# Kernel tuning notes

Hardware: AMD Instinct MI355X
Metric: run time of the kernel (lower is better)

Reference implementation:

```python
import jax, jax.numpy as jnp
import numpy as np

B, S, H, NH = 2, 2048, 1024, 16
HD = H // NH  # 64
EPS = 1e-5


def setup_inputs() -> dict:
    key = jax.random.key(0)
    ks = jax.random.split(key, 4)
    return {
        "hidden_states": jax.random.normal(ks[0], (B, S, H), dtype=jnp.float32),
        "W_attn": jax.random.normal(ks[1], (H, 3 * H), dtype=jnp.float32) * (1.0 / np.sqrt(H)),
        "b_attn": jnp.zeros((3 * H,), dtype=jnp.float32),
        "W_proj": jax.random.normal(ks[2], (H, H), dtype=jnp.float32) * (1.0 / np.sqrt(H)),
        "b_proj": jnp.zeros((H,), dtype=jnp.float32),
        "q_gamma": jnp.ones((HD,), dtype=jnp.float32),
        "q_beta": jnp.zeros((HD,), dtype=jnp.float32),
        "k_gamma": jnp.ones((HD,), dtype=jnp.float32),
        "k_beta": jnp.zeros((HD,), dtype=jnp.float32),
    }


def _layernorm(x, gamma, beta):
    mu = jnp.mean(x, axis=-1, keepdims=True)
    var = jnp.mean(jnp.square(x - mu), axis=-1, keepdims=True)
    return (x - mu) * jax.lax.rsqrt(var + EPS) * gamma + beta


def reference(hidden_states, W_attn, b_attn, W_proj, b_proj, q_gamma, q_beta, k_gamma, k_beta):
    b, s, h = hidden_states.shape
    qkv = hidden_states @ W_attn + b_attn  # [B,S,3H]
    q, k, v = jnp.split(qkv, 3, axis=-1)
    # [B,S,H] -> [B,NH,S,HD]
    def to_heads(t):
        return t.reshape(b, s, NH, HD).transpose(0, 2, 1, 3)
    q, k, v = to_heads(q), to_heads(k), to_heads(v)
    # QK LayerNorm over head_dim
    q = _layernorm(q, q_gamma, q_beta)
    k = _layernorm(k, k_gamma, k_beta)
    scale = HD ** (-0.5)
    scores = jnp.einsum("bhqd,bhkd->bhqk", q, k) * scale
    causal = jnp.tril(jnp.ones((s, s), dtype=bool))
    mask_value = jnp.finfo(scores.dtype).min
    scores = jnp.where(causal, scores, mask_value)
    attn = jax.nn.softmax(scores.astype(jnp.float32), axis=-1).astype(q.dtype)
    out = jnp.einsum("bhqk,bhkd->bhqd", attn, v)
    out = out.transpose(0, 2, 1, 3).reshape(b, s, h)
    out = out @ W_proj + b_proj
    return out
```

## Files before the change

### kernel.cpp

```cpp
#include <hip/hip_runtime.h>
#include <hip/hip_bf16.h>

typedef __bf16 bf16x8 __attribute__((ext_vector_type(8)));
typedef float f32x4 __attribute__((ext_vector_type(4)));

#define EPS 1e-5f
#define QSCALE 0.18033688011112042f

__device__ __forceinline__ unsigned short f2bf(float f) {
  union { float f; unsigned int i; } c; c.f = f;
  unsigned int r = c.i + 0x7FFFu + ((c.i >> 16) & 1u);
  return (unsigned short)(r >> 16);
}

__global__ __launch_bounds__(256) void transpose_f32_bf16(
    const float* __restrict__ in, unsigned short* __restrict__ out,
    int R, int C)
{
  __shared__ __align__(16) unsigned short S[64 * 72];
  const int t = threadIdx.x;
  const int r = t >> 2, c4 = (t & 3) * 16;
  const int rt0 = blockIdx.y * 64, ct0 = blockIdx.x * 64;

  {
    long base = (long)(rt0 + r) * C + ct0 + c4;
    float4 a = *(const float4*)&in[base];
    float4 b = *(const float4*)&in[base + 4];
    float4 c = *(const float4*)&in[base + 8];
    float4 d = *(const float4*)&in[base + 12];
    unsigned short v[16] = {f2bf(a.x), f2bf(a.y), f2bf(a.z), f2bf(a.w),
                            f2bf(b.x), f2bf(b.y), f2bf(b.z), f2bf(b.w),
                            f2bf(c.x), f2bf(c.y), f2bf(c.z), f2bf(c.w),
                            f2bf(d.x), f2bf(d.y), f2bf(d.z), f2bf(d.w)};
    *(uint4*)&S[r * 72 + c4]     = *(uint4*)&v[0];
    *(uint4*)&S[r * 72 + c4 + 8] = *(uint4*)&v[8];
  }
  __syncthreads();

  unsigned short tmp[16];
#pragma unroll
  for (int j = 0; j < 16; j++) tmp[j] = S[(c4 + j) * 72 + r];
  *(uint4*)&out[(long)(ct0 + r) * R + rt0 + c4]     = *(uint4*)&tmp[0];
  *(uint4*)&out[(long)(ct0 + r) * R + rt0 + c4 + 8] = *(uint4*)&tmp[8];
}

__global__ __launch_bounds__(256) void convert_f32_bf16(
    const float* __restrict__ in, unsigned short* __restrict__ out)
{
  long i = ((long)blockIdx.x * 256 + threadIdx.x) * 16;
  float4 a = *(const float4*)&in[i];
  float4 b = *(const float4*)&in[i + 4];
  float4 c = *(const float4*)&in[i + 8];
  float4 d = *(const float4*)&in[i + 12];
  unsigned short v[16] = {f2bf(a.x), f2bf(a.y), f2bf(a.z), f2bf(a.w),
                          f2bf(b.x), f2bf(b.y), f2bf(b.z), f2bf(b.w),
                          f2bf(c.x), f2bf(c.y), f2bf(c.z), f2bf(c.w),
                          f2bf(d.x), f2bf(d.y), f2bf(d.z), f2bf(d.w)};
  *(uint4*)&out[i]     = *(uint4*)&v[0];
  *(uint4*)&out[i + 8] = *(uint4*)&v[8];
}

__global__ __launch_bounds__(256) void qkv_ln_kernel(
    const float* __restrict__ Xf,
    const unsigned short* __restrict__ Xbf, int use_xbf,
    const unsigned short* __restrict__ WT,
    const float* __restrict__ bias,
    const float* __restrict__ qg, const float* __restrict__ qb,
    const float* __restrict__ kg, const float* __restrict__ kb,
    unsigned short* __restrict__ Qws, unsigned short* __restrict__ Kws)
{
  __shared__ __align__(16) unsigned short As[2][128 * 32];
  __shared__ __align__(16) unsigned short Bs[2][128 * 32];

  const int tid = threadIdx.x;
  const int w = tid >> 6, lane = tid & 63, quad = lane >> 4, l15 = lane & 15;
  const int mh = w & 1, nh = w >> 1;
  const int n0 = blockIdx.x * 128, m0 = blockIdx.y * 128;

  f32x4 acc[4][4];
#pragma unroll
  for (int i = 0; i < 4; i++)
#pragma unroll
    for (int j = 0; j < 4; j++) acc[i][j] = (f32x4){0.f, 0.f, 0.f, 0.f};

  const int sr2 = tid >> 1, sh2 = (tid & 1) * 16;

  if (use_xbf) {
    long xo = (long)(m0 + sr2) * 1024 + sh2;
    *(uint4*)&As[0][sr2 * 32 + sh2]     = *(const uint4*)&Xbf[xo];
    *(uint4*)&As[0][sr2 * 32 + sh2 + 8] = *(const uint4*)&Xbf[xo + 8];
  } else {
    long xo = (long)(m0 + sr2) * 1024 + sh2;
    float4 a0 = *(const float4*)&Xf[xo];
    float4 a1 = *(const float4*)&Xf[xo + 4];
    float4 a2 = *(const float4*)&Xf[xo + 8];
    float4 a3 = *(const float4*)&Xf[xo + 12];
    unsigned short v[16] = {f2bf(a0.x), f2bf(a0.y), f2bf(a0.z), f2bf(a0.w),
                            f2bf(a1.x), f2bf(a1.y), f2bf(a1.z), f2bf(a1.w),
                            f2bf(a2.x), f2bf(a2.y), f2bf(a2.z), f2bf(a2.w),
                            f2bf(a3.x), f2bf(a3.y), f2bf(a3.z), f2bf(a3.w)};
    *(uint4*)&As[0][sr2 * 32 + sh2]     = *(uint4*)&v[0];
    *(uint4*)&As[0][sr2 * 32 + sh2 + 8] = *(uint4*)&v[8];
  }
  {
    long wo = (long)(n0 + sr2) * 1024 + sh2;
    *(uint4*)&Bs[0][sr2 * 32 + sh2]     = *(const uint4*)&WT[wo];
    *(uint4*)&Bs[0][sr2 * 32 + sh2 + 8] = *(const uint4*)&WT[wo + 8];
  }
  __syncthreads();

  int buf = 0;
  for (int kt = 0; kt < 1024; kt += 32) {
    const int nbuf = buf ^ 1;
    const bool pf = (kt + 32) < 1024;
    uint4 xv0, xv1, wv0, wv1;
    float4 a0, a1, a2, a3;
    if (pf) {
      if (use_xbf) {
        long xo = (long)(m0 + sr2) * 1024 + kt + 32 + sh2;
        xv0 = *(const uint4*)&Xbf[xo];
        xv1 = *(const uint4*)&Xbf[xo + 8];
      } else {
        long xo = (long)(m0 + sr2) * 1024 + kt + 32 + sh2;
        a0 = *(const float4*)&Xf[xo];
        a1 = *(const float4*)&Xf[xo + 4];
        a2 = *(const float4*)&Xf[xo + 8];
        a3 = *(const float4*)&Xf[xo + 12];
      }
      long wo = (long)(n0 + sr2) * 1024 + kt + 32 + sh2;
      wv0 = *(const uint4*)&WT[wo];
      wv1 = *(const uint4*)&WT[wo + 8];
    }

    bf16x8 af[4], bfr[4];
#pragma unroll
    for (int mq = 0; mq < 4; mq++)
      af[mq] = *(const bf16x8*)&As[buf][(mh * 64 + mq * 16 + l15) * 32 + quad * 8];
#pragma unroll
    for (int nq = 0; nq < 4; nq++)
      bfr[nq] = *(const bf16x8*)&Bs[buf][(nh * 64 + nq * 16 + l15) * 32 + quad * 8];
#pragma unroll
    for (int mq = 0; mq < 4; mq++)
#pragma unroll
      for (int nq = 0; nq < 4; nq++)
        acc[mq][nq] = __builtin_amdgcn_mfma_f32_16x16x32_bf16(af[mq], bfr[nq], acc[mq][nq], 0, 0, 0);

    if (pf) {
      if (use_xbf) {
        *(uint4*)&As[nbuf][sr2 * 32 + sh2]     = xv0;
        *(uint4*)&As[nbuf][sr2 * 32 + sh2 + 8] = xv1;
      } else {
        unsigned short v[16] = {f2bf(a0.x), f2bf(a0.y), f2bf(a0.z), f2bf(a0.w),
                                f2bf(a1.x), f2bf(a1.y), f2bf(a1.z), f2bf(a1.w),
                                f2bf(a2.x), f2bf(a2.y), f2bf(a2.z), f2bf(a2.w),
                                f2bf(a3.x), f2bf(a3.y), f2bf(a3.z), f2bf(a3.w)};
        *(uint4*)&As[nbuf][sr2 * 32 + sh2]     = *(uint4*)&v[0];
        *(uint4*)&As[nbuf][sr2 * 32 + sh2 + 8] = *(uint4*)&v[8];
      }
      *(uint4*)&Bs[nbuf][sr2 * 32 + sh2]     = wv0;
      *(uint4*)&Bs[nbuf][sr2 * 32 + sh2 + 8] = wv1;
    }
    __syncthreads();
    buf = nbuf;
  }

#pragma unroll
  for (int nq = 0; nq < 4; nq++) {
    float bv = bias[n0 + nh * 64 + nq * 16 + l15];
#pragma unroll
    for (int mq = 0; mq < 4; mq++)
#pragma unroll
      for (int rr = 0; rr < 4; rr++) acc[mq][nq][rr] += bv;
  }

  const int g = (n0 >> 6) + nh;
  const bool isQ = g < 16;

  {
    float gv[4], bev[4];
#pragma unroll
    for (int nq = 0; nq < 4; nq++) {
      int d = nq * 16 + l15;
      gv[nq]  = isQ ? qg[d] : kg[d];
      bev[nq] = isQ ? qb[d] : kb[d];
      if (isQ) { gv[nq] *= QSCALE; bev[nq] *= QSCALE; }
    }
#pragma unroll
    for (int mq = 0; mq < 4; mq++)
#pragma unroll
      for (int rr = 0; rr < 4; rr++) {
        float s  = acc[mq][0][rr] + acc[mq][1][rr] + acc[mq][2][rr] + acc[mq][3][rr];
        float s2 = acc[mq][0][rr]*acc[mq][0][rr] + acc[mq][1][rr]*acc[mq][1][rr]
                 + acc[mq][2][rr]*acc[mq][2][rr] + acc[mq][3][rr]*acc[mq][3][rr];
#pragma unroll
        for (int off = 1; off < 16; off <<= 1) {
          s  += __shfl_xor(s,  off, 64);
          s2 += __shfl_xor(s2, off, 64);
        }
        float mu   = s * (1.0f / 64.0f);
        float var  = fmaxf(s2 * (1.0f / 64.0f) - mu * mu, 0.f);
        float rstd = rsqrtf(var + EPS);
#pragma unroll
        for (int nq = 0; nq < 4; nq++)
          acc[mq][nq][rr] = (acc[mq][nq][rr] - mu) * rstd * gv[nq] + bev[nq];
      }
  }

  unsigned short* dst = isQ ? Qws : Kws;
  const int head = isQ ? g : g - 16;

#pragma unroll
  for (int mq = 0; mq < 4; mq++)
#pragma unroll
    for (int rr = 0; rr < 4; rr++) {
      int m = m0 + mh * 64 + mq * 16 + quad * 4 + rr;
      int b = m >> 11, s = m & 2047;
      long base = ((long)((b * 16 + head) * 2048 + s)) * 64;
#pragma unroll
      for (int nq = 0; nq < 4; nq++)
        dst[base + nq * 16 + l15] = f2bf(acc[mq][nq][rr]);
    }
}

__global__ __launch_bounds__(256) void vt_kernel(
    const float* __restrict__ Xf,
    const unsigned short* __restrict__ Xbf, int use_xbf,
    const unsigned short* __restrict__ WvT,
    const float* __restrict__ bias,
    unsigned short* __restrict__ Vt)
{
  __shared__ __align__(16) unsigned short As[2][128 * 32];
  __shared__ __align__(16) unsigned short Bs[2][128 * 32];

  const int tid = threadIdx.x;
  const int w = tid >> 6, lane = tid & 63, quad = lane >> 4, l15 = lane & 15;
  const int mh = w & 1, nh = w >> 1;
  const int n0 = blockIdx.x * 128, m0 = blockIdx.y * 128, bz = blockIdx.z;
  const long xrow0 = (long)bz * 2048;

  f32x4 acc[4][4];
#pragma unroll
  for (int i = 0; i < 4; i++)
#pragma unroll
    for (int j = 0; j < 4; j++) acc[i][j] = (f32x4){0.f, 0.f, 0.f, 0.f};

  const int sr2 = tid >> 1, sh2 = (tid & 1) * 16;

  {
    long wo = (long)(m0 + sr2) * 1024 + sh2;
    *(uint4*)&As[0][sr2 * 32 + sh2]     = *(const uint4*)&WvT[wo];
    *(uint4*)&As[0][sr2 * 32 + sh2 + 8] = *(const uint4*)&WvT[wo + 8];
  }
  if (use_xbf) {
    long xo = (xrow0 + n0 + sr2) * 1024 + sh2;
    *(uint4*)&Bs[0][sr2 * 32 + sh2]     = *(const uint4*)&Xbf[xo];
    *(uint4*)&Bs[0][sr2 * 32 + sh2 + 8] = *(const uint4*)&Xbf[xo + 8];
  } else {
    long xo = (xrow0 + n0 + sr2) * 1024 + sh2;
    float4 a0 = *(const float4*)&Xf[xo];
    float4 a1 = *(const float4*)&Xf[xo + 4];
    float4 a2 = *(const float4*)&Xf[xo + 8];
    float4 a3 = *(const float4*)&Xf[xo + 12];
    unsigned short v[16] = {f2bf(a0.x), f2bf(a0.y), f2bf(a0.z), f2bf(a0.w),
                            f2bf(a1.x), f2bf(a1.y), f2bf(a1.z), f2bf(a1.w),
                            f2bf(a2.x), f2bf(a2.y), f2bf(a2.z), f2bf(a2.w),
                            f2bf(a3.x), f2bf(a3.y), f2bf(a3.z), f2bf(a3.w)};
    *(uint4*)&Bs[0][sr2 * 32 + sh2]     = *(uint4*)&v[0];
    *(uint4*)&Bs[0][sr2 * 32 + sh2 + 8] = *(uint4*)&v[8];
  }
  __syncthreads();

  int buf = 0;
  for (int kt = 0; kt < 1024; kt += 32) {
    const int nbuf = buf ^ 1;
    const bool pf = (kt + 32) < 1024;
    uint4 wv0, wv1, xv0, xv1;
    float4 a0, a1, a2, a3;
    if (pf) {
      long wo = (long)(m0 + sr2) * 1024 + kt + 32 + sh2;
      wv0 = *(const uint4*)&WvT[wo];
      wv1 = *(const uint4*)&WvT[wo + 8];
      long xo = (xrow0 + n0 + sr2) * 1024 + kt + 32 + sh2;
      if (use_xbf) {
        xv0 = *(const uint4*)&Xbf[xo];
        xv1 = *(const uint4*)&Xbf[xo + 8];
      } else {
        a0 = *(const float4*)&Xf[xo];
        a1 = *(const float4*)&Xf[xo + 4];
        a2 = *(const float4*)&Xf[xo + 8];
        a3 = *(const float4*)&Xf[xo + 12];
      }
    }

    bf16x8 af[4], bfr[4];
#pragma unroll
    for (int mq = 0; mq < 4; mq++)
      af[mq] = *(const bf16x8*)&As[buf][(mh * 64 + mq * 16 + l15) * 32 + quad * 8];
#pragma unroll
    for (int nq = 0; nq < 4; nq++)
      bfr[nq] = *(const bf16x8*)&Bs[buf][(nh * 64 + nq * 16 + l15) * 32 + quad * 8];
#pragma unroll
    for (int mq = 0; mq < 4; mq++)
#pragma unroll
      for (int nq = 0; nq < 4; nq++)
        acc[mq][nq] = __builtin_amdgcn_mfma_f32_16x16x32_bf16(af[mq], bfr[nq], acc[mq][nq], 0, 0, 0);

    if (pf) {
      *(uint4*)&As[nbuf][sr2 * 32 + sh2]     = wv0;
      *(uint4*)&As[nbuf][sr2 * 32 + sh2 + 8] = wv1;
      if (use_xbf) {
        *(uint4*)&Bs[nbuf][sr2 * 32 + sh2]     = xv0;
        *(uint4*)&Bs[nbuf][sr2 * 32 + sh2 + 8] = xv1;
      } else {
        unsigned short v[16] = {f2bf(a0.x), f2bf(a0.y), f2bf(a0.z), f2bf(a0.w),
                                f2bf(a1.x), f2bf(a1.y), f2bf(a1.z), f2bf(a1.w),
                                f2bf(a2.x), f2bf(a2.y), f2bf(a2.z), f2bf(a2.w),
                                f2bf(a3.x), f2bf(a3.y), f2bf(a3.z), f2bf(a3.w)};
        *(uint4*)&Bs[nbuf][sr2 * 32 + sh2]     = *(uint4*)&v[0];
        *(uint4*)&Bs[nbuf][sr2 * 32 + sh2 + 8] = *(uint4*)&v[8];
      }
    }
    __syncthreads();
    buf = nbuf;
  }

  const long outb = (long)bz * 2097152;
#pragma unroll
  for (int mq = 0; mq < 4; mq++)
#pragma unroll
    for (int rr = 0; rr < 4; rr++) {
      int m = m0 + mh * 64 + mq * 16 + quad * 4 + rr;
      float bv = bias[2048 + m];
#pragma unroll
      for (int nq = 0; nq < 4; nq++) {
        int n = n0 + nh * 64 + nq * 16 + l15;
        Vt[outb + (long)m * 2048 + n] = f2bf(acc[mq][nq][rr] + bv);
      }
    }
}

__global__ __launch_bounds__(256, 6) void attn_kernel(
    unsigned short* __restrict__ Qws,
    const unsigned short* __restrict__ Kws,
    const unsigned short* __restrict__ Vt)
{
  __shared__ __align__(16) unsigned short Ks[64 * 72];
  __shared__ __align__(16) unsigned short VTs[64 * 72];
  __shared__ __align__(16) unsigned short Ps[64 * 64];

  const int tid = threadIdx.x;
  const int w = tid >> 6, lane = tid & 63, quad = lane >> 4, l15 = lane & 15;
  const int bh = blockIdx.y;
  const int qt = ((bh >> 3) & 1) ? blockIdx.x : (31 - blockIdx.x);
  const int qbase = qt * 64;
  const long bhoff = (long)bh * 2048 * 64;
  const long bhv   = (long)bh * 131072;
  const int jmax = qt + 1;

  const int sr = tid >> 2, sc = (tid & 3) * 16;

  *(uint4*)&Ps[sr * 64 + sc]     = *(const uint4*)&Qws[bhoff + (qbase + sr) * 64 + sc];
  *(uint4*)&Ps[sr * 64 + sc + 8] = *(const uint4*)&Qws[bhoff + (qbase + sr) * 64 + sc + 8];
  *(uint4*)&Ks[sr * 72 + sc]      = *(const uint4*)&Kws[bhoff + sr * 64 + sc];
  *(uint4*)&Ks[sr * 72 + sc + 8]  = *(const uint4*)&Kws[bhoff + sr * 64 + sc + 8];
  *(uint4*)&VTs[sr * 72 + sc]     = *(const uint4*)&Vt[bhv + sr * 2048 + sc];
  *(uint4*)&VTs[sr * 72 + sc + 8] = *(const uint4*)&Vt[bhv + sr * 2048 + sc + 8];
  __syncthreads();

  const bf16x8 qf0 = *(const bf16x8*)&Ps[(w * 16 + l15) * 64 + quad * 8];
  const bf16x8 qf1 = *(const bf16x8*)&Ps[(w * 16 + l15) * 64 + 32 + quad * 8];

  bf16x8 ones;
  {
    union { unsigned short u[8]; bf16x8 v; } c;
#pragma unroll
    for (int i = 0; i < 8; i++) c.u[i] = 0x3F80u;
    ones = c.v;
  }

  f32x4 o[4], osum;
#pragma unroll
  for (int i = 0; i < 4; i++) o[i] = (f32x4){0.f, 0.f, 0.f, 0.f};
  osum = (f32x4){0.f, 0.f, 0.f, 0.f};

  const int sw = ((l15 >> 2) & 3) << 4;
  const int pc0 = (quad * 8) ^ sw;
  const int pc1 = (32 + quad * 8) ^ sw;

  for (int j = 0; j < jmax; j++) {
    const int kb = j * 64;
    const bool pf = (j + 1) < jmax;
    uint4 pk0, pk1, pv0, pv1;
    if (pf) {
      const int kb1 = kb + 64;
      pk0 = *(const uint4*)&Kws[bhoff + (kb1 + sr) * 64 + sc];
      pk1 = *(const uint4*)&Kws[bhoff + (kb1 + sr) * 64 + sc + 8];
      pv0 = *(const uint4*)&Vt[bhv + sr * 2048 + kb1 + sc];
      pv1 = *(const uint4*)&Vt[bhv + sr * 2048 + kb1 + sc + 8];
    }

    f32x4 sacc[4];
#pragma unroll
    for (int i = 0; i < 4; i++) sacc[i] = (f32x4){0.f, 0.f, 0.f, 0.f};
#pragma unroll
    for (int nt = 0; nt < 4; nt++) {
      bf16x8 kf0 = *(const bf16x8*)&Ks[(nt * 16 + l15) * 72 + quad * 8];
      bf16x8 kf1 = *(const bf16x8*)&Ks[(nt * 16 + l15) * 72 + 32 + quad * 8];
      sacc[nt] = __builtin_amdgcn_mfma_f32_16x16x32_bf16(qf0, kf0, sacc[nt], 0, 0, 0);
      sacc[nt] = __builtin_amdgcn_mfma_f32_16x16x32_bf16(qf1, kf1, sacc[nt], 0, 0, 0);
    }

    const bool domask = (j == qt);
#pragma unroll
    for (int nt = 0; nt < 4; nt++)
#pragma unroll
      for (int rr = 0; rr < 4; rr++) {
        float p = exp2f(sacc[nt][rr]);
        if (domask) {
          int kcol = kb + nt * 16 + l15;
          int qrow = qbase + w * 16 + quad * 4 + rr;
          if (kcol > qrow) p = 0.f;
        }
        sacc[nt][rr] = p;
      }

#pragma unroll
    for (int rr = 0; rr < 4; rr++)
#pragma unroll
      for (int nt = 0; nt < 4; nt++)
        Ps[(w * 16 + quad * 4 + rr) * 64 + (((nt ^ quad) & 3) * 16 + l15)]
            = f2bf(sacc[nt][rr]);

    bf16x8 pfr0 = *(const bf16x8*)&Ps[(w * 16 + l15) * 64 + pc0];
    bf16x8 pfr1 = *(const bf16x8*)&Ps[(w * 16 + l15) * 64 + pc1];

    osum = __builtin_amdgcn_mfma_f32_16x16x32_bf16(pfr0, ones, osum, 0, 0, 0);
    osum = __builtin_amdgcn_mfma_f32_16x16x32_bf16(pfr1, ones, osum, 0, 0, 0);
#pragma unroll
    for (int dt = 0; dt < 4; dt++) {
      bf16x8 vf0 = *(const bf16x8*)&VTs[(dt * 16 + l15) * 72 + quad * 8];
      bf16x8 vf1 = *(const bf16x8*)&VTs[(dt * 16 + l15) * 72 + 32 + quad * 8];
      o[dt] = __builtin_amdgcn_mfma_f32_16x16x32_bf16(pfr0, vf0, o[dt], 0, 0, 0);
      o[dt] = __builtin_amdgcn_mfma_f32_16x16x32_bf16(pfr1, vf1, o[dt], 0, 0, 0);
    }

    if (pf) {
      __syncthreads();
      *(uint4*)&Ks[sr * 72 + sc]      = pk0;
      *(uint4*)&Ks[sr * 72 + sc + 8]  = pk1;
      *(uint4*)&VTs[sr * 72 + sc]     = pv0;
      *(uint4*)&VTs[sr * 72 + sc + 8] = pv1;
      __syncthreads();
    }
  }

#pragma unroll
  for (int rr = 0; rr < 4; rr++) {
    float inv = 1.0f / osum[rr];
    int row = qbase + w * 16 + quad * 4 + rr;
    long base = bhoff + (long)row * 64;
#pragma unroll
    for (int dt = 0; dt < 4; dt++)
      Qws[base + dt * 16 + l15] = f2bf(o[dt][rr] * inv);
  }
}

__global__ __launch_bounds__(256) void proj_kernel(
    const unsigned short* __restrict__ AQ,
    const unsigned short* __restrict__ WT,
    const float* __restrict__ bias,
    float* __restrict__ Out)
{
  __shared__ __align__(16) unsigned short As[2][128 * 32];
  __shared__ __align__(16) unsigned short Bs[2][128 * 32];

  const int tid = threadIdx.x;
  const int w = tid >> 6, lane = tid & 63, quad = lane >> 4, l15 = lane & 15;
  const int mh = w & 1, nh = w >> 1;
  const int n0 = blockIdx.x * 128, m0 = blockIdx.y * 128;

  f32x4 acc[4][4];
#pragma unroll
  for (int i = 0; i < 4; i++)
#pragma unroll
    for (int j = 0; j < 4; j++) acc[i][j] = (f32x4){0.f, 0.f, 0.f, 0.f};

  const int sr2 = tid >> 1, sh2 = (tid & 1) * 16;
  const int m = m0 + sr2, b = m >> 11, s = m & 2047;

  {
    const int h = sh2 >> 6, d = sh2 & 63;
    long ao = ((long)((b * 16 + h) * 2048 + s)) * 64 + d;
    *(uint4*)&As[0][sr2 * 32 + sh2]     = *(const uint4*)&AQ[ao];
    *(uint4*)&As[0][sr2 * 32 + sh2 + 8] = *(const uint4*)&AQ[ao + 8];
    long wo = (long)(n0 + sr2) * 1024 + sh2;
    *(uint4*)&Bs[0][sr2 * 32 + sh2]     = *(const uint4*)&WT[wo];
    *(uint4*)&Bs[0][sr2 * 32 + sh2 + 8] = *(const uint4*)&WT[wo + 8];
  }
  __syncthreads();

  int buf = 0;
  for (int kt = 0; kt < 1024; kt += 32) {
    const int nbuf = buf ^ 1;
    const bool pf = (kt + 32) < 1024;
    uint4 av0, av1, wv0, wv1;
    if (pf) {
      const int k = kt + 32 + sh2, h = k >> 6, d = k & 63;
      long ao = ((long)((b * 16 + h) * 2048 + s)) * 64 + d;
      av0 = *(const uint4*)&AQ[ao];
      av1 = *(const uint4*)&AQ[ao + 8];
      long wo = (long)(n0 + sr2) * 1024 + kt + 32 + sh2;
      wv0 = *(const uint4*)&WT[wo];
      wv1 = *(const uint4*)&WT[wo + 8];
    }

    bf16x8 af[4], bfr[4];
#pragma unroll
    for (int mq = 0; mq < 4; mq++)
      af[mq] = *(const bf16x8*)&As[buf][(mh * 64 + mq * 16 + l15) * 32 + quad * 8];
#pragma unroll
    for (int nq = 0; nq < 4; nq++)
      bfr[nq] = *(const bf16x8*)&Bs[buf][(nh * 64 + nq * 16 + l15) * 32 + quad * 8];
#pragma unroll
    for (int mq = 0; mq < 4; mq++)
#pragma unroll
      for (int nq = 0; nq < 4; nq++)
        acc[mq][nq] = __builtin_amdgcn_mfma_f32_16x16x32_bf16(af[mq], bfr[nq], acc[mq][nq], 0, 0, 0);

    if (pf) {
      *(uint4*)&As[nbuf][sr2 * 32 + sh2]     = av0;
      *(uint4*)&As[nbuf][sr2 * 32 + sh2 + 8] = av1;
      *(uint4*)&Bs[nbuf][sr2 * 32 + sh2]     = wv0;
      *(uint4*)&Bs[nbuf][sr2 * 32 + sh2 + 8] = wv1;
    }
    __syncthreads();
    buf = nbuf;
  }

#pragma unroll
  for (int nq = 0; nq < 4; nq++) {
    int n = n0 + nh * 64 + nq * 16 + l15;
    float bv = bias[n];
#pragma unroll
    for (int mq = 0; mq < 4; mq++)
#pragma unroll
      for (int rr = 0; rr < 4; rr++) {
        int mm = m0 + mh * 64 + mq * 16 + quad * 4 + rr;
        Out[(long)mm * 1024 + n] = acc[mq][nq][rr] + bv;
      }
  }
}

extern "C" void kernel_launch(void* const* d_in, const int* in_sizes, int n_in,
                              void* d_out, int out_size, void* d_ws, size_t ws_size,
                              hipStream_t stream) {
  const float* X  = (const float*)d_in[0];
  const float* Wa = (const float*)d_in[1];
  const float* ba = (const float*)d_in[2];
  const float* Wp = (const float*)d_in[3];
  const float* bp = (const float*)d_in[4];
  const float* qg = (const float*)d_in[5];
  const float* qb = (const float*)d_in[6];
  const float* kg = (const float*)d_in[7];
  const float* kb = (const float*)d_in[8];

  const long per = 2L * 16 * 2048 * 64;
  unsigned short* ws  = (unsigned short*)d_ws;
  unsigned short* Qws = ws;
  unsigned short* Kws = Qws + per;
  unsigned short* Vt  = Kws + per;

  const bool big = ws_size >= (size_t)(5L * per * 2);
  unsigned short *Xbf, *WaT, *WpT;
  if (big) {
    Xbf = Vt + per;
    WaT = Xbf + per;
    WpT = WaT + 3072L * 1024;
  } else {
    Xbf = Qws;
    WaT = Vt + per;
    WpT = WaT + 3072L * 1024;
  }
  unsigned short* WvT = WaT + 2048L * 1024;

  transpose_f32_bf16<<<dim3(48, 16), 256, 0, stream>>>(Wa, WaT, 1024, 3072);
  transpose_f32_bf16<<<dim3(16, 16), 256, 0, stream>>>(Wp, WpT, 1024, 1024);
  if (big) convert_f32_bf16<<<1024, 256, 0, stream>>>(X, Xbf);
  qkv_ln_kernel<<<dim3(16, 32), 256, 0, stream>>>(X, Xbf, big ? 1 : 0, WaT, ba,
                                                  qg, qb, kg, kb, Qws, Kws);
  vt_kernel<<<dim3(16, 8, 2), 256, 0, stream>>>(X, Xbf, big ? 1 : 0, WvT, ba, Vt);
  attn_kernel<<<dim3(32, 32), 256, 0, stream>>>(Qws, Kws, Vt);
  proj_kernel<<<dim3(8, 32), 256, 0, stream>>>(Qws, WpT, bp, (float*)d_out);
}
```

Baseline: 222.1 us.

## Use direct global-to-LDS loads in GEMMs and 128-row query tiles in attention

The three GEMM kernels now stage their bf16 tiles with global_load_lds DMA straight into shared memory, replacing the register round-trip through uint4 loads and LDS stores. The attention kernel now handles 128 query rows per block (two 16-row MFMA subtiles per wave) with a swizzled Q staging buffer. This halves the attention grid and reuses each K/V tile across twice as many queries. The trade-offs are more registers, the loss of the occupancy hint and coarser causal load balance, and the async LDS loads rely on the existing barriers for ordering.

```diff
diff --git a/kernel.cpp b/kernel.cpp
--- a/kernel.cpp
+++ b/kernel.cpp
@@ -12,6 +12,11 @@
   unsigned int r = c.i + 0x7FFFu + ((c.i >> 16) & 1u);
   return (unsigned short)(r >> 16);
 }
+
+#define GLOAD_LDS16(g, s)                                                  \
+  __builtin_amdgcn_global_load_lds(                                        \
+      (const __attribute__((address_space(1))) unsigned int*)(g),          \
+      (__attribute__((address_space(3))) unsigned int*)(s), 16, 0, 0)
 
 __global__ __launch_bounds__(256) void transpose_f32_bf16(
     const float* __restrict__ in, unsigned short* __restrict__ out,
@@ -83,13 +88,17 @@
 #pragma unroll
     for (int j = 0; j < 4; j++) acc[i][j] = (f32x4){0.f, 0.f, 0.f, 0.f};
 
+  const int srow = lane >> 2, soff = (lane & 3) * 8;
   const int sr2 = tid >> 1, sh2 = (tid & 1) * 16;
 
-  if (use_xbf) {
-    long xo = (long)(m0 + sr2) * 1024 + sh2;
-    *(uint4*)&As[0][sr2 * 32 + sh2]     = *(const uint4*)&Xbf[xo];
-    *(uint4*)&As[0][sr2 * 32 + sh2 + 8] = *(const uint4*)&Xbf[xo + 8];
-  } else {
+#pragma unroll
+  for (int i = 0; i < 2; i++) {
+    const int rr0 = w * 32 + i * 16;
+    GLOAD_LDS16(WT + (long)(n0 + rr0 + srow) * 1024 + soff, &Bs[0][rr0 * 32]);
+    if (use_xbf)
+      GLOAD_LDS16(Xbf + (long)(m0 + rr0 + srow) * 1024 + soff, &As[0][rr0 * 32]);
+  }
+  if (!use_xbf) {
     long xo = (long)(m0 + sr2) * 1024 + sh2;
     float4 a0 = *(const float4*)&Xf[xo];
     float4 a1 = *(const float4*)&Xf[xo + 4];
@@ -102,34 +111,30 @@
     *(uint4*)&As[0][sr2 * 32 + sh2]     = *(uint4*)&v[0];
     *(uint4*)&As[0][sr2 * 32 + sh2 + 8] = *(uint4*)&v[8];
   }
-  {
-    long wo = (long)(n0 + sr2) * 1024 + sh2;
-    *(uint4*)&Bs[0][sr2 * 32 + sh2]     = *(const uint4*)&WT[wo];
-    *(uint4*)&Bs[0][sr2 * 32 + sh2 + 8] = *(const uint4*)&WT[wo + 8];
-  }
   __syncthreads();
 
   int buf = 0;
   for (int kt = 0; kt < 1024; kt += 32) {
     const int nbuf = buf ^ 1;
     const bool pf = (kt + 32) < 1024;
-    uint4 xv0, xv1, wv0, wv1;
     float4 a0, a1, a2, a3;
     if (pf) {
-      if (use_xbf) {
-        long xo = (long)(m0 + sr2) * 1024 + kt + 32 + sh2;
-        xv0 = *(const uint4*)&Xbf[xo];
-        xv1 = *(const uint4*)&Xbf[xo + 8];
-      } else {
+#pragma unroll
+      for (int i = 0; i < 2; i++) {
+        const int rr0 = w * 32 + i * 16;
+        GLOAD_LDS16(WT + (long)(n0 + rr0 + srow) * 1024 + kt + 32 + soff,
+                    &Bs[nbuf][rr0 * 32]);
+        if (use_xbf)
+          GLOAD_LDS16(Xbf + (long)(m0 + rr0 + srow) * 1024 + kt + 32 + soff,
+                      &As[nbuf][rr0 * 32]);
+      }
+      if (!use_xbf) {
         long xo = (long)(m0 + sr2) * 1024 + kt + 32 + sh2;
         a0 = *(const float4*)&Xf[xo];
         a1 = *(const float4*)&Xf[xo + 4];
         a2 = *(const float4*)&Xf[xo + 8];
         a3 = *(const float4*)&Xf[xo + 12];
       }
-      long wo = (long)(n0 + sr2) * 1024 + kt + 32 + sh2;
-      wv0 = *(const uint4*)&WT[wo];
-      wv1 = *(const uint4*)&WT[wo + 8];
     }
 
     bf16x8 af[4], bfr[4];
@@ -145,20 +150,13 @@
       for (int nq = 0; nq < 4; nq++)
         acc[mq][nq] = __builtin_amdgcn_mfma_f32_16x16x32_bf16(af[mq], bfr[nq], acc[mq][nq], 0, 0, 0);
 
-    if (pf) {
-      if (use_xbf) {
-        *(uint4*)&As[nbuf][sr2 * 32 + sh2]     = xv0;
-        *(uint4*)&As[nbuf][sr2 * 32 + sh2 + 8] = xv1;
-      } else {
-        unsigned short v[16] = {f2bf(a0.x), f2bf(a0.y), f2bf(a0.z), f2bf(a0.w),
-                                f2bf(a1.x), f2bf(a1.y), f2bf(a1.z), f2bf(a1.w),
-                                f2bf(a2.x), f2bf(a2.y), f2bf(a2.z), f2bf(a2.w),
-                                f2bf(a3.x), f2bf(a3.y), f2bf(a3.z), f2bf(a3.w)};
-        *(uint4*)&As[nbuf][sr2 * 32 + sh2]     = *(uint4*)&v[0];
-        *(uint4*)&As[nbuf][sr2 * 32 + sh2 + 8] = *(uint4*)&v[8];
-      }
-      *(uint4*)&Bs[nbuf][sr2 * 32 + sh2]     = wv0;
-      *(uint4*)&Bs[nbuf][sr2 * 32 + sh2 + 8] = wv1;
+    if (pf && !use_xbf) {
+      unsigned short v[16] = {f2bf(a0.x), f2bf(a0.y), f2bf(a0.z), f2bf(a0.w),
+                              f2bf(a1.x), f2bf(a1.y), f2bf(a1.z), f2bf(a1.w),
+                              f2bf(a2.x), f2bf(a2.y), f2bf(a2.z), f2bf(a2.w),
+                              f2bf(a3.x), f2bf(a3.y), f2bf(a3.z), f2bf(a3.w)};
+      *(uint4*)&As[nbuf][sr2 * 32 + sh2]     = *(uint4*)&v[0];
+      *(uint4*)&As[nbuf][sr2 * 32 + sh2 + 8] = *(uint4*)&v[8];
     }
     __syncthreads();
     buf = nbuf;
@@ -244,18 +242,17 @@
 #pragma unroll
     for (int j = 0; j < 4; j++) acc[i][j] = (f32x4){0.f, 0.f, 0.f, 0.f};
 
+  const int srow = lane >> 2, soff = (lane & 3) * 8;
   const int sr2 = tid >> 1, sh2 = (tid & 1) * 16;
 
-  {
-    long wo = (long)(m0 + sr2) * 1024 + sh2;
-    *(uint4*)&As[0][sr2 * 32 + sh2]     = *(const uint4*)&WvT[wo];
-    *(uint4*)&As[0][sr2 * 32 + sh2 + 8] = *(const uint4*)&WvT[wo + 8];
-  }
-  if (use_xbf) {
-    long xo = (xrow0 + n0 + sr2) * 1024 + sh2;
-    *(uint4*)&Bs[0][sr2 * 32 + sh2]     = *(const uint4*)&Xbf[xo];
-    *(uint4*)&Bs[0][sr2 * 32 + sh2 + 8] = *(const uint4*)&Xbf[xo + 8];
-  } else {
+#pragma unroll
+  for (int i = 0; i < 2; i++) {
+    const int rr0 = w * 32 + i * 16;
+    GLOAD_LDS16(WvT + (long)(m0 + rr0 + srow) * 1024 + soff, &As[0][rr0 * 32]);
+    if (use_xbf)
+      GLOAD_LDS16(Xbf + (xrow0 + n0 + rr0 + srow) * 1024 + soff, &Bs[0][rr0 * 32]);
+  }
+  if (!use_xbf) {
     long xo = (xrow0 + n0 + sr2) * 1024 + sh2;
     float4 a0 = *(const float4*)&Xf[xo];
     float4 a1 = *(const float4*)&Xf[xo + 4];
@@ -274,17 +271,19 @@
   for (int kt = 0; kt < 1024; kt += 32) {
     const int nbuf = buf ^ 1;
     const bool pf = (kt + 32) < 1024;
-    uint4 wv0, wv1, xv0, xv1;
     float4 a0, a1, a2, a3;
     if (pf) {
-      long wo = (long)(m0 + sr2) * 1024 + kt + 32 + sh2;
-      wv0 = *(const uint4*)&WvT[wo];
-      wv1 = *(const uint4*)&WvT[wo + 8];
-      long xo = (xrow0 + n0 + sr2) * 1024 + kt + 32 + sh2;
-      if (use_xbf) {
-        xv0 = *(const uint4*)&Xbf[xo];
-        xv1 = *(const uint4*)&Xbf[xo + 8];
-      } else {
+#pragma unroll
+      for (int i = 0; i < 2; i++) {
+        const int rr0 = w * 32 + i * 16;
+        GLOAD_LDS16(WvT + (long)(m0 + rr0 + srow) * 1024 + kt + 32 + soff,
+                    &As[nbuf][rr0 * 32]);
+        if (use_xbf)
+          GLOAD_LDS16(Xbf + (xrow0 + n0 + rr0 + srow) * 1024 + kt + 32 + soff,
+                      &Bs[nbuf][rr0 * 32]);
+      }
+      if (!use_xbf) {
+        long xo = (xrow0 + n0 + sr2) * 1024 + kt + 32 + sh2;
         a0 = *(const float4*)&Xf[xo];
         a1 = *(const float4*)&Xf[xo + 4];
         a2 = *(const float4*)&Xf[xo + 8];
@@ -305,20 +304,13 @@
       for (int nq = 0; nq < 4; nq++)
         acc[mq][nq] = __builtin_amdgcn_mfma_f32_16x16x32_bf16(af[mq], bfr[nq], acc[mq][nq], 0, 0, 0);
 
-    if (pf) {
-      *(uint4*)&As[nbuf][sr2 * 32 + sh2]     = wv0;
-      *(uint4*)&As[nbuf][sr2 * 32 + sh2 + 8] = wv1;
-      if (use_xbf) {
-        *(uint4*)&Bs[nbuf][sr2 * 32 + sh2]     = xv0;
-        *(uint4*)&Bs[nbuf][sr2 * 32 + sh2 + 8] = xv1;
-      } else {
-        unsigned short v[16] = {f2bf(a0.x), f2bf(a0.y), f2bf(a0.z), f2bf(a0.w),
-                                f2bf(a1.x), f2bf(a1.y), f2bf(a1.z), f2bf(a1.w),
-                                f2bf(a2.x), f2bf(a2.y), f2bf(a2.z), f2bf(a2.w),
-                                f2bf(a3.x), f2bf(a3.y), f2bf(a3.z), f2bf(a3.w)};
-        *(uint4*)&Bs[nbuf][sr2 * 32 + sh2]     = *(uint4*)&v[0];
-        *(uint4*)&Bs[nbuf][sr2 * 32 + sh2 + 8] = *(uint4*)&v[8];
-      }
+    if (pf && !use_xbf) {
+      unsigned short v[16] = {f2bf(a0.x), f2bf(a0.y), f2bf(a0.z), f2bf(a0.w),
+                              f2bf(a1.x), f2bf(a1.y), f2bf(a1.z), f2bf(a1.w),
+                              f2bf(a2.x), f2bf(a2.y), f2bf(a2.z), f2bf(a2.w),
+                              f2bf(a3.x), f2bf(a3.y), f2bf(a3.z), f2bf(a3.w)};
+      *(uint4*)&Bs[nbuf][sr2 * 32 + sh2]     = *(uint4*)&v[0];
+      *(uint4*)&Bs[nbuf][sr2 * 32 + sh2 + 8] = *(uint4*)&v[8];
     }
     __syncthreads();
     buf = nbuf;
@@ -339,36 +331,48 @@
     }
 }
 
-__global__ __launch_bounds__(256, 6) void attn_kernel(
+__global__ __launch_bounds__(256) void attn_kernel(
     unsigned short* __restrict__ Qws,
     const unsigned short* __restrict__ Kws,
     const unsigned short* __restrict__ Vt)
 {
   __shared__ __align__(16) unsigned short Ks[64 * 72];
   __shared__ __align__(16) unsigned short VTs[64 * 72];
-  __shared__ __align__(16) unsigned short Ps[64 * 64];
+  __shared__ __align__(16) unsigned short Ps[128 * 64];
 
   const int tid = threadIdx.x;
   const int w = tid >> 6, lane = tid & 63, quad = lane >> 4, l15 = lane & 15;
   const int bh = blockIdx.y;
-  const int qt = ((bh >> 3) & 1) ? blockIdx.x : (31 - blockIdx.x);
-  const int qbase = qt * 64;
+  const int qt2 = (bh < 16) ? (15 - blockIdx.x) : blockIdx.x;
+  const int qbase = qt2 * 128;
   const long bhoff = (long)bh * 2048 * 64;
   const long bhv   = (long)bh * 131072;
-  const int jmax = qt + 1;
+  const int jmax = 2 * qt2 + 2;
 
   const int sr = tid >> 2, sc = (tid & 3) * 16;
-
-  *(uint4*)&Ps[sr * 64 + sc]     = *(const uint4*)&Qws[bhoff + (qbase + sr) * 64 + sc];
-  *(uint4*)&Ps[sr * 64 + sc + 8] = *(const uint4*)&Qws[bhoff + (qbase + sr) * 64 + sc + 8];
+  const int qr = tid >> 1, qc = (tid & 1) * 32;
+  const int qsw = ((qr >> 2) & 3) << 4;
+
+#pragma unroll
+  for (int c = 0; c < 32; c += 8)
+    *(uint4*)&Ps[qr * 64 + (((qc + c) ^ qsw))] =
+        *(const uint4*)&Qws[bhoff + (qbase + qr) * 64 + qc + c];
   *(uint4*)&Ks[sr * 72 + sc]      = *(const uint4*)&Kws[bhoff + sr * 64 + sc];
   *(uint4*)&Ks[sr * 72 + sc + 8]  = *(const uint4*)&Kws[bhoff + sr * 64 + sc + 8];
   *(uint4*)&VTs[sr * 72 + sc]     = *(const uint4*)&Vt[bhv + sr * 2048 + sc];
   *(uint4*)&VTs[sr * 72 + sc + 8] = *(const uint4*)&Vt[bhv + sr * 2048 + sc + 8];
   __syncthreads();
 
-  const bf16x8 qf0 = *(const bf16x8*)&Ps[(w * 16 + l15) * 64 + quad * 8];
-  const bf16x8 qf1 = *(const bf16x8*)&Ps[(w * 16 + l15) * 64 + 32 + quad * 8];
+  const int sw = ((l15 >> 2) & 3) << 4;
+  const int pc0 = (quad * 8) ^ sw;
+  const int pc1 = (32 + quad * 8) ^ sw;
+
+  bf16x8 qf[2][2];
+#pragma unroll
+  for (int mq = 0; mq < 2; mq++) {
+    qf[mq][0] = *(const bf16x8*)&Ps[(w * 32 + mq * 16 + l15) * 64 + pc0];
+    qf[mq][1] = *(const bf16x8*)&Ps[(w * 32 + mq * 16 + l15) * 64 + pc1];
+  }
 
   bf16x8 ones;
   {
@@ -378,14 +382,13 @@
     ones = c.v;
   }
 
-  f32x4 o[4], osum;
-#pragma unroll
-  for (int i = 0; i < 4; i++) o[i] = (f32x4){0.f, 0.f, 0.f, 0.f};
-  osum = (f32x4){0.f, 0.f, 0.f, 0.f};
-
-  const int sw = ((l15 >> 2) & 3) << 4;
-  const int pc0 = (quad * 8) ^ sw;
-  const int pc1 = (32 + quad * 8) ^ sw;
+  f32x4 o[2][4], osum[2];
+#pragma unroll
+  for (int mq = 0; mq < 2; mq++) {
+#pragma unroll
+    for (int i = 0; i < 4; i++) o[mq][i] = (f32x4){0.f, 0.f, 0.f, 0.f};
+    osum[mq] = (f32x4){0.f, 0.f, 0.f, 0.f};
+  }
 
   for (int j = 0; j < jmax; j++) {
     const int kb = j * 64;
@@ -399,49 +402,68 @@
       pv1 = *(const uint4*)&Vt[bhv + sr * 2048 + kb1 + sc + 8];
     }
 
-    f32x4 sacc[4];
-#pragma unroll
-    for (int i = 0; i < 4; i++) sacc[i] = (f32x4){0.f, 0.f, 0.f, 0.f};
+    f32x4 sacc[2][4];
+#pragma unroll
+    for (int mq = 0; mq < 2; mq++)
+#pragma unroll
+      for (int i = 0; i < 4; i++) sacc[mq][i] = (f32x4){0.f, 0.f, 0.f, 0.f};
 #pragma unroll
     for (int nt = 0; nt < 4; nt++) {
       bf16x8 kf0 = *(const bf16x8*)&Ks[(nt * 16 + l15) * 72 + quad * 8];
       bf16x8 kf1 = *(const bf16x8*)&Ks[(nt * 16 + l15) * 72 + 32 + quad * 8];
-      sacc[nt] = __builtin_amdgcn_mfma_f32_16x16x32_bf16(qf0, kf0, sacc[nt], 0, 0, 0);
-      sacc[nt] = __builtin_amdgcn_mfma_f32_16x16x32_bf16(qf1, kf1, sacc[nt], 0, 0, 0);
-    }
-
-    const bool domask = (j == qt);
-#pragma unroll
-    for (int nt = 0; nt < 4; nt++)
-#pragma unroll
-      for (int rr = 0; rr < 4; rr++) {
-        float p = exp2f(sacc[nt][rr]);
-        if (domask) {
-          int kcol = kb + nt * 16 + l15;
-          int qrow = qbase + w * 16 + quad * 4 + rr;
-          if (kcol > qrow) p = 0.f;
+#pragma unroll
+      for (int mq = 0; mq < 2; mq++) {
+        sacc[mq][nt] = __builtin_amdgcn_mfma_f32_16x16x32_bf16(qf[mq][0], kf0, sacc[mq][nt], 0, 0, 0);
+        sacc[mq][nt] = __builtin_amdgcn_mfma_f32_16x16x32_bf16(qf[mq][1], kf1, sacc[mq][nt], 0, 0, 0);
+      }
+    }
+
+    const bool domask = (j >= 2 * qt2);
+#pragma unroll
+    for (int mq = 0; mq < 2; mq++)
+#pragma unroll
+      for (int nt = 0; nt < 4; nt++)
+#pragma unroll
+        for (int rr = 0; rr < 4; rr++) {
+          float p = exp2f(sacc[mq][nt][rr]);
+          if (domask) {
+            int kcol = kb + nt * 16 + l15;
+            int qrow = qbase + w * 32 + mq * 16 + quad * 4 + rr;
+            if (kcol > qrow) p = 0.f;
+          }
+          sacc[mq][nt][rr] = p;
         }
-        sacc[nt][rr] = p;
-      }
-
-#pragma unroll
-    for (int rr = 0; rr < 4; rr++)
-#pragma unroll
-      for (int nt = 0; nt < 4; nt++)
-        Ps[(w * 16 + quad * 4 + rr) * 64 + (((nt ^ quad) & 3) * 16 + l15)]
-            = f2bf(sacc[nt][rr]);
-
-    bf16x8 pfr0 = *(const bf16x8*)&Ps[(w * 16 + l15) * 64 + pc0];
-    bf16x8 pfr1 = *(const bf16x8*)&Ps[(w * 16 + l15) * 64 + pc1];
-
-    osum = __builtin_amdgcn_mfma_f32_16x16x32_bf16(pfr0, ones, osum, 0, 0, 0);
-    osum = __builtin_amdgcn_mfma_f32_16x16x32_bf16(pfr1, ones, osum, 0, 0, 0);
+
+#pragma unroll
+    for (int mq = 0; mq < 2; mq++)
+#pragma unroll
+      for (int rr = 0; rr < 4; rr++)
+#pragma unroll
+        for (int nt = 0; nt < 4; nt++)
+          Ps[(w * 32 + mq * 16 + quad * 4 + rr) * 64 + (((nt ^ quad) & 3) * 16 + l15)]
+              = f2bf(sacc[mq][nt][rr]);
+
+    bf16x8 pfr[2][2];
+#pragma unroll
+    for (int mq = 0; mq < 2; mq++) {
+      pfr[mq][0] = *(const bf16x8*)&Ps[(w * 32 + mq * 16 + l15) * 64 + pc0];
+      pfr[mq][1] = *(const bf16x8*)&Ps[(w * 32 + mq * 16 + l15) * 64 + pc1];
+    }
+
+#pragma unroll
+    for (int mq = 0; mq < 2; mq++) {
+      osum[mq] = __builtin_amdgcn_mfma_f32_16x16x32_bf16(pfr[mq][0], ones, osum[mq], 0, 0, 0);
+      osum[mq] = __builtin_amdgcn_mfma_f32_16x16x32_bf16(pfr[mq][1], ones, osum[mq], 0, 0, 0);
+    }
 #pragma unroll
     for (int dt = 0; dt < 4; dt++) {
       bf16x8 vf0 = *(const bf16x8*)&VTs[(dt * 16 + l15) * 72 + quad * 8];
       bf16x8 vf1 = *(const bf16x8*)&VTs[(dt * 16 + l15) * 72 + 32 + quad * 8];
-      o[dt] = __builtin_amdgcn_mfma_f32_16x16x32_bf16(pfr0, vf0, o[dt], 0, 0, 0);
-      o[dt] = __builtin_amdgcn_mfma_f32_16x16x32_bf16(pfr1, vf1, o[dt], 0, 0, 0);
+#pragma unroll
+      for (int mq = 0; mq < 2; mq++) {
+        o[mq][dt] = __builtin_amdgcn_mfma_f32_16x16x32_bf16(pfr[mq][0], vf0, o[mq][dt], 0, 0, 0);
+        o[mq][dt] = __builtin_amdgcn_mfma_f32_16x16x32_bf16(pfr[mq][1], vf1, o[mq][dt], 0, 0, 0);
+      }
     }
 
     if (pf) {
@@ -455,14 +477,16 @@
   }
 
 #pragma unroll
-  for (int rr = 0; rr < 4; rr++) {
-    float inv = 1.0f / osum[rr];
-    int row = qbase + w * 16 + quad * 4 + rr;
-    long base = bhoff + (long)row * 64;
-#pragma unroll
-    for (int dt = 0; dt < 4; dt++)
-      Qws[base + dt * 16 + l15] = f2bf(o[dt][rr] * inv);
-  }
+  for (int mq = 0; mq < 2; mq++)
+#pragma unroll
+    for (int rr = 0; rr < 4; rr++) {
+      float inv = 1.0f / osum[mq][rr];
+      int row = qbase + w * 32 + mq * 16 + quad * 4 + rr;
+      long base = bhoff + (long)row * 64;
+#pragma unroll
+      for (int dt = 0; dt < 4; dt++)
+        Qws[base + dt * 16 + l15] = f2bf(o[mq][dt][rr] * inv);
+    }
 }
 
 __global__ __launch_bounds__(256) void proj_kernel(
@@ -485,17 +509,14 @@
 #pragma unroll
     for (int j = 0; j < 4; j++) acc[i][j] = (f32x4){0.f, 0.f, 0.f, 0.f};
 
-  const int sr2 = tid >> 1, sh2 = (tid & 1) * 16;
-  const int m = m0 + sr2, b = m >> 11, s = m & 2047;
-
-  {
-    const int h = sh2 >> 6, d = sh2 & 63;
-    long ao = ((long)((b * 16 + h) * 2048 + s)) * 64 + d;
-    *(uint4*)&As[0][sr2 * 32 + sh2]     = *(const uint4*)&AQ[ao];
-    *(uint4*)&As[0][sr2 * 32 + sh2 + 8] = *(const uint4*)&AQ[ao + 8];
-    long wo = (long)(n0 + sr2) * 1024 + sh2;
-    *(uint4*)&Bs[0][sr2 * 32 + sh2]     = *(const uint4*)&WT[wo];
-    *(uint4*)&Bs[0][sr2 * 32 + sh2 + 8] = *(const uint4*)&WT[wo + 8];
+  const int srow = lane >> 2, soff = (lane & 3) * 8;
+
+#pragma unroll
+  for (int i = 0; i < 2; i++) {
+    const int rr0 = w * 32 + i * 16;
+    const int m = m0 + rr0 + srow, b = m >> 11, s = m & 2047;
+    GLOAD_LDS16(AQ + ((long)(b * 16) * 2048 + s) * 64 + soff, &As[0][rr0 * 32]);
+    GLOAD_LDS16(WT + (long)(n0 + rr0 + srow) * 1024 + soff, &Bs[0][rr0 * 32]);
   }
   __syncthreads();
 
@@ -503,15 +524,17 @@
   for (int kt = 0; kt < 1024; kt += 32) {
     const int nbuf = buf ^ 1;
     const bool pf = (kt + 32) < 1024;
-    uint4 av0, av1, wv0, wv1;
     if (pf) {
-      const int k = kt + 32 + sh2, h = k >> 6, d = k & 63;
-      long ao = ((long)((b * 16 + h) * 2048 + s)) * 64 + d;
-      av0 = *(const uint4*)&AQ[ao];
-      av1 = *(const uint4*)&AQ[ao + 8];
-      long wo = (long)(n0 + sr2) * 1024 + kt + 32 + sh2;
-      wv0 = *(const uint4*)&WT[wo];
-      wv1 = *(const uint4*)&WT[wo + 8];
+      const int k = kt + 32, h = k >> 6, d0 = k & 63;
+#pragma unroll
+      for (int i = 0; i < 2; i++) {
+        const int rr0 = w * 32 + i * 16;
+        const int m = m0 + rr0 + srow, b = m >> 11, s = m & 2047;
+        GLOAD_LDS16(AQ + ((long)((b * 16 + h) * 2048) + s) * 64 + d0 + soff,
+                    &As[nbuf][rr0 * 32]);
+        GLOAD_LDS16(WT + (long)(n0 + rr0 + srow) * 1024 + k + soff,
+                    &Bs[nbuf][rr0 * 32]);
+      }
     }
 
     bf16x8 af[4], bfr[4];
@@ -526,13 +549,6 @@
 #pragma unroll
       for (int nq = 0; nq < 4; nq++)
         acc[mq][nq] = __builtin_amdgcn_mfma_f32_16x16x32_bf16(af[mq], bfr[nq], acc[mq][nq], 0, 0, 0);
-
-    if (pf) {
-      *(uint4*)&As[nbuf][sr2 * 32 + sh2]     = av0;
-      *(uint4*)&As[nbuf][sr2 * 32 + sh2 + 8] = av1;
-      *(uint4*)&Bs[nbuf][sr2 * 32 + sh2]     = wv0;
-      *(uint4*)&Bs[nbuf][sr2 * 32 + sh2 + 8] = wv1;
-    }
     __syncthreads();
     buf = nbuf;
   }
@@ -589,6 +605,6 @@
   qkv_ln_kernel<<<dim3(16, 32), 256, 0, stream>>>(X, Xbf, big ? 1 : 0, WaT, ba,
                                                   qg, qb, kg, kb, Qws, Kws);
   vt_kernel<<<dim3(16, 8, 2), 256, 0, stream>>>(X, Xbf, big ? 1 : 0, WvT, ba, Vt);
-  attn_kernel<<<dim3(32, 32), 256, 0, stream>>>(Qws, Kws, Vt);
+  attn_kernel<<<dim3(16, 32), 256, 0, stream>>>(Qws, Kws, Vt);
   proj_kernel<<<dim3(8, 32), 256, 0, stream>>>(Qws, WpT, bp, (float*)d_out);
 }
```

Result: slower. 235.8 us (+6.2%).
